# Kernel tuning notes

Measured on AMD Instinct MI355X. Metric: run time of the kernel, lower is better.

Reference implementation:

```python
import jax, jax.numpy as jnp
import numpy as np

B = 8192      # batch tokens
D = 2048      # d_model
N = 32768
K = 32        # top-k sparsity


def setup_inputs() -> dict:
    key = jax.random.key(0)
    k1, k2 = jax.random.split(key, 2)
    x = jax.random.normal(k1, (B, D), dtype=jnp.float32)
    # encoder weight [N, D] (nn.Linear(d_model, n_dirs).weight)
    enc_w = jax.random.normal(k2, (N, D), dtype=jnp.float32) * (1.0 / np.sqrt(D))
    # decoder initialized as encoder transpose, then unit-normed columns
    dec_w = enc_w.T  # [D, N]
    dec_w = dec_w / jnp.linalg.norm(dec_w, axis=0, keepdims=True)
    pre_bias = jnp.zeros((D,), dtype=jnp.float32)
    latent_bias = jnp.zeros((N,), dtype=jnp.float32)
    return {"x": x, "enc_w": enc_w, "dec_w": dec_w,
            "pre_bias": pre_bias, "latent_bias": latent_bias}


def reference(x, enc_w, dec_w, pre_bias, latent_bias):
    # latents_pre_act = (x - pre_bias) @ enc_w.T + latent_bias
    xc = x - pre_bias                                   # [B, D]
    latents = xc @ enc_w.T + latent_bias                # [B, N]
    # single-shard sharded_topk == plain top-k (sh_comm is None -> k_in = k)
    vals, inds = jax.lax.top_k(latents, K)              # [B, K]
    vals = jax.nn.relu(vals)
    # sparse decode: gather only the K active decoder columns per token
    cols = dec_w.T[inds]                                # [B, K, D]
    recons = jnp.einsum('bk,bkd->bd', vals, cols) + pre_bias  # [B, D]
    return recons
```

## Files before the change

### kernel.cpp

```cpp
#include <hip/hip_runtime.h>
#include <stdint.h>

#define B_TOK 8192
#define DMODEL 2048
#define NDIR 32768
#define KTOP 32
#define CAP 512
#define NREF 64
#define THRESH 2.5f

typedef __attribute__((ext_vector_type(8))) short short8;
typedef __attribute__((ext_vector_type(4))) float f32x4;

__device__ __forceinline__ uint16_t f2bf(float f) {
  uint32_t u = __float_as_uint(f);
  u = (u + 0x7fffu + ((u >> 16) & 1u)) >> 16;
  return (uint16_t)u;
}
__device__ __forceinline__ float bf2f(uint32_t u) { return __uint_as_float(u << 16); }

__device__ __forceinline__ void async_load16(const void* g, void* l) {
  __builtin_amdgcn_global_load_lds(
      (const __attribute__((address_space(1))) unsigned int*)g,
      (__attribute__((address_space(3))) unsigned int*)l, 16, 0, 0);
}

__global__ void prep_x_k(const float* __restrict__ x, const float* __restrict__ pre_bias,
                         uint16_t* __restrict__ xh) {
  size_t i = ((size_t)blockIdx.x * blockDim.x + threadIdx.x) * 4;
  float4 v = *reinterpret_cast<const float4*>(x + i);
  int d = (int)(i & (DMODEL - 1));
  float4 p = *reinterpret_cast<const float4*>(pre_bias + d);
  ushort4 o;
  o.x = f2bf(v.x - p.x); o.y = f2bf(v.y - p.y);
  o.z = f2bf(v.z - p.z); o.w = f2bf(v.w - p.w);
  *reinterpret_cast<ushort4*>(xh + i) = o;
}

__global__ void prep_w_k(const float* __restrict__ w, uint16_t* __restrict__ wh) {
  size_t i = ((size_t)blockIdx.x * blockDim.x + threadIdx.x) * 4;
  float4 v = *reinterpret_cast<const float4*>(w + i);
  ushort4 o;
  o.x = f2bf(v.x); o.y = f2bf(v.y); o.z = f2bf(v.z); o.w = f2bf(v.w);
  *reinterpret_cast<ushort4*>(wh + i) = o;
}

__global__ __launch_bounds__(512, 2) void gemm_topk(
    const uint16_t* __restrict__ xh, const uint16_t* __restrict__ wh,
    const float* __restrict__ latent_bias,
    float* __restrict__ cand_val, int* __restrict__ cand_idx, int* __restrict__ cand_cnt) {
  __shared__ char smem[131072];
  const int tid = threadIdx.x;
  const int w = tid >> 6, l = tid & 63;
  const int lr = l & 15, g = l >> 4;
  const int wm_w = (w >> 2) * 128;
  const int wn_w = (w & 3) * 64;

  int bid = blockIdx.x;
  int swz = (bid & 7) * 512 + (bid >> 3);
  const int bm = swz >> 7, bn = swz & 127;
  const int m0i = bm * 256, n0i = bn * 256;

  const char* Agb = (const char*)xh + (size_t)m0i * 4096;
  const char* Bgb = (const char*)wh + (size_t)n0i * 4096;

  const int key = (lr & 7) << 4;
  const int cx0 = (g << 4) ^ key;
  const int cx1 = (64 | (g << 4)) ^ key;

  const char* ArdBase = smem + (wm_w >> 7) * 16384;
  const char* BrdBase = smem + 32768 + (wn_w >> 7) * 16384;
  const int bhr = wn_w & 64;

  f32x4 acc[8][4] = {};
  short8 a[8], b[8];

  auto stage = [&](const char* grow0, char* dst) {
#pragma unroll
    for (int inst = 0; inst < 2; ++inst) {
      int o = inst * 8192 + tid * 16;
      int row = o >> 7;
      int cb = (o & 127) ^ ((row & 7) << 4);
      async_load16(grow0 + (size_t)row * 4096 + cb, dst + inst * 8192 + (tid >> 6) * 1024);
    }
  };

  const int NT = DMODEL / 64;

  stage(Agb, smem);
  stage(Agb + 524288, smem + 16384);
  stage(Bgb, smem + 32768);
  stage(Bgb + 524288, smem + 49152);
  stage(Bgb + 128, smem + 65536 + 32768);
  stage(Bgb + 524288 + 128, smem + 65536 + 49152);
  asm volatile("s_waitcnt vmcnt(4)" ::: "memory");
  __builtin_amdgcn_s_barrier();

  for (int t = 0; t < NT; ++t) {
    const int p = t & 1;
    const char* At = ArdBase + p * 65536;
    const char* Bt = BrdBase + p * 65536;
    char* SA = smem + ((t + 1) & 1) * 65536;
    char* SB = smem + p * 65536 + 32768;
    const char* Ag = Agb + (size_t)(t + 1) * 128;
    const char* Bg = Bgb + (size_t)(t + 2) * 128;
    const bool s1 = (t + 1 < NT), s2 = (t + 2 < NT);

#pragma unroll
    for (int f = 0; f < 4; ++f) {
      const char* rA = At + (f * 16 + lr) * 128;
      a[f * 2 + 0] = *(const short8*)(rA + cx0);
      a[f * 2 + 1] = *(const short8*)(rA + cx1);
    }
#pragma unroll
    for (int f = 0; f < 2; ++f) {
      const char* rB = Bt + (bhr + f * 16 + lr) * 128;
      b[f * 2 + 0] = *(const short8*)(rB + cx0);
      b[f * 2 + 1] = *(const short8*)(rB + cx1);
    }
    if (s1) stage(Ag, SA);
    __builtin_amdgcn_s_barrier();
    asm volatile("s_waitcnt lgkmcnt(0)" ::: "memory");
    __builtin_amdgcn_s_setprio(1);
#pragma unroll
    for (int fm = 0; fm < 4; ++fm)
#pragma unroll
      for (int fn = 0; fn < 2; ++fn)
#pragma unroll
        for (int kk = 0; kk < 2; ++kk)
          acc[fm][fn] = __builtin_amdgcn_mfma_f32_16x16x32_bf16(a[fm * 2 + kk], b[fn * 2 + kk],
                                                                acc[fm][fn], 0, 0, 0);
    __builtin_amdgcn_s_setprio(0);
    __builtin_amdgcn_s_barrier();

#pragma unroll
    for (int f = 2; f < 4; ++f) {
      const char* rB = Bt + (bhr + f * 16 + lr) * 128;
      b[f * 2 + 0] = *(const short8*)(rB + cx0);
      b[f * 2 + 1] = *(const short8*)(rB + cx1);
    }
    if (s1) stage(Ag + 524288, SA + 16384);
    __builtin_amdgcn_s_barrier();
    asm volatile("s_waitcnt lgkmcnt(0)" ::: "memory");
    __builtin_amdgcn_s_setprio(1);
#pragma unroll
    for (int fm = 0; fm < 4; ++fm)
#pragma unroll
      for (int fn = 2; fn < 4; ++fn)
#pragma unroll
        for (int kk = 0; kk < 2; ++kk)
          acc[fm][fn] = __builtin_amdgcn_mfma_f32_16x16x32_bf16(a[fm * 2 + kk], b[fn * 2 + kk],
                                                                acc[fm][fn], 0, 0, 0);
    __builtin_amdgcn_s_setprio(0);
    __builtin_amdgcn_s_barrier();

#pragma unroll
    for (int f = 0; f < 4; ++f) {
      const char* rA = At + ((f + 4) * 16 + lr) * 128;
      a[f * 2 + 0] = *(const short8*)(rA + cx0);
      a[f * 2 + 1] = *(const short8*)(rA + cx1);
    }
    if (s2) stage(Bg, SB);
    __builtin_amdgcn_s_barrier();
    asm volatile("s_waitcnt lgkmcnt(0)" ::: "memory");
    __builtin_amdgcn_s_setprio(1);
#pragma unroll
    for (int fm = 4; fm < 8; ++fm)
#pragma unroll
      for (int fn = 2; fn < 4; ++fn)
#pragma unroll
        for (int kk = 0; kk < 2; ++kk)
          acc[fm][fn] = __builtin_amdgcn_mfma_f32_16x16x32_bf16(a[(fm - 4) * 2 + kk],
                                                                b[fn * 2 + kk], acc[fm][fn], 0, 0, 0);
    __builtin_amdgcn_s_setprio(0);
    __builtin_amdgcn_s_barrier();

    if (s2) stage(Bg + 524288, SB + 16384);
    if (t < NT - 2)
      asm volatile("s_waitcnt vmcnt(4)" ::: "memory");
    else
      asm volatile("s_waitcnt vmcnt(0)" ::: "memory");
    __builtin_amdgcn_s_barrier();
    __builtin_amdgcn_s_setprio(1);
#pragma unroll
    for (int fm = 4; fm < 8; ++fm)
#pragma unroll
      for (int fn = 0; fn < 2; ++fn)
#pragma unroll
        for (int kk = 0; kk < 2; ++kk)
          acc[fm][fn] = __builtin_amdgcn_mfma_f32_16x16x32_bf16(a[(fm - 4) * 2 + kk],
                                                                b[fn * 2 + kk], acc[fm][fn], 0, 0, 0);
    __builtin_amdgcn_s_setprio(0);
    __builtin_amdgcn_s_barrier();
  }

#pragma unroll
  for (int fn = 0; fn < 4; ++fn) {
    int gn = n0i + wn_w + fn * 16 + lr;
    float lb = latent_bias[gn];
#pragma unroll
    for (int fm = 0; fm < 8; ++fm) {
      int gmb = m0i + wm_w + fm * 16 + g * 4;
#pragma unroll
      for (int j = 0; j < 4; ++j) {
        float v = acc[fm][fn][j] + lb;
        if (v > THRESH) {
          int gm = gmb + j;
          int pos = atomicAdd(&cand_cnt[gm], 1);
          if (pos < CAP) {
            cand_val[(size_t)gm * CAP + pos] = v;
            cand_idx[(size_t)gm * CAP + pos] = gn;
          }
        }
      }
    }
  }
}

__global__ __launch_bounds__(256) void select_refine(
    const float* __restrict__ x, const float* __restrict__ pre_bias,
    const float* __restrict__ enc_w, const float* __restrict__ latent_bias,
    const float* __restrict__ cand_val, const int* __restrict__ cand_idx,
    const int* __restrict__ cand_cnt,
    float* __restrict__ sel_val, int* __restrict__ sel_idx) {
  __shared__ float sv[CAP];
  __shared__ int si[CAP];
  __shared__ float xc[DMODEL];
  __shared__ double red[4];
  __shared__ double rv[NREF];
  __shared__ int ri[NREF];

  const int row = blockIdx.x, tid = threadIdx.x;

  for (int d = tid; d < DMODEL; d += 256)
    xc[d] = x[(size_t)row * DMODEL + d] - pre_bias[d];

  int c = cand_cnt[row];
  if (c > CAP) c = CAP;
  for (int i = tid; i < CAP; i += 256) {
    if (i < c) {
      sv[i] = cand_val[(size_t)row * CAP + i];
      si[i] = cand_idx[(size_t)row * CAP + i];
    } else {
      sv[i] = -1e30f;
      si[i] = 0x7fffffff;
    }
  }

  for (int k = 2; k <= CAP; k <<= 1) {
    for (int j = k >> 1; j > 0; j >>= 1) {
      __syncthreads();
      int i = ((tid & ~(j - 1)) << 1) | (tid & (j - 1));
      int p = i | j;
      bool up = ((i & k) == 0);
      float va = sv[i], vb = sv[p];
      int ia = si[i], ib = si[p];
      bool aFirst = (va > vb) || (va == vb && ia < ib);
      if (up ? (!aFirst) : aFirst) {
        sv[i] = vb; sv[p] = va; si[i] = ib; si[p] = ia;
      }
    }
  }
  __syncthreads();

  const int nref = c < NREF ? c : NREF;
  for (int jc = 0; jc < NREF; ++jc) {
    if (jc < nref) {
      int n = si[jc];
      const float* wrow = enc_w + (size_t)n * DMODEL;
      double s = 0.0;
      for (int d = tid; d < DMODEL; d += 256)
        s += (double)xc[d] * (double)wrow[d];
#pragma unroll
      for (int off = 32; off > 0; off >>= 1)
        s += __shfl_down(s, off);
      if ((tid & 63) == 0) red[tid >> 6] = s;
      __syncthreads();
      if (tid == 0) {
        rv[jc] = red[0] + red[1] + red[2] + red[3] + (double)latent_bias[n];
        ri[jc] = n;
      }
      __syncthreads();
    } else {
      if (tid == 0) { rv[jc] = -1e300; ri[jc] = 0x7fffffff; }
    }
  }
  __syncthreads();

  for (int k = 2; k <= NREF; k <<= 1) {
    for (int j = k >> 1; j > 0; j >>= 1) {
      __syncthreads();
      if (tid < NREF / 2) {
        int i = ((tid & ~(j - 1)) << 1) | (tid & (j - 1));
        int p = i | j;
        bool up = ((i & k) == 0);
        double va = rv[i], vb = rv[p];
        int ia = ri[i], ib = ri[p];
        bool aFirst = (va > vb) || (va == vb && ia < ib);
        if (up ? (!aFirst) : aFirst) {
          rv[i] = vb; rv[p] = va; ri[i] = ib; ri[p] = ia;
        }
      }
    }
  }
  __syncthreads();
  if (tid < KTOP) {
    double v = rv[tid];
    int n = ri[tid];
    float f = (n < NDIR && v > 0.0) ? (float)v : 0.0f;
    sel_val[(size_t)row * KTOP + tid] = f;
    sel_idx[(size_t)row * KTOP + tid] = (n < NDIR) ? n : 0;
  }
}

__global__ void transpose_dec(const float* __restrict__ dec_w, uint16_t* __restrict__ dec_wt) {
  __shared__ float tile[32][33];
  int n0 = blockIdx.x * 32, d0 = blockIdx.y * 32;
  int tx = threadIdx.x, ty = threadIdx.y;
#pragma unroll
  for (int i = 0; i < 4; ++i)
    tile[ty + i * 8][tx] = dec_w[(size_t)(d0 + ty + i * 8) * NDIR + n0 + tx];
  __syncthreads();
#pragma unroll
  for (int i = 0; i < 4; ++i)
    dec_wt[(size_t)(n0 + ty + i * 8) * DMODEL + d0 + tx] = f2bf(tile[tx][ty + i * 8]);
}

__global__ __launch_bounds__(256) void decode_k(
    const uint16_t* __restrict__ dec_wt, const float* __restrict__ sel_val,
    const int* __restrict__ sel_idx, const float* __restrict__ pre_bias,
    float* __restrict__ out) {
  __shared__ float vs[KTOP];
  __shared__ int isx[KTOP];
  const int b = blockIdx.x, tid = threadIdx.x;
  if (tid < KTOP) {
    vs[tid] = sel_val[(size_t)b * KTOP + tid];
    isx[tid] = sel_idx[(size_t)b * KTOP + tid];
  }
  __syncthreads();
  const int d = tid * 8;
  float acc[8];
  float4 p0 = *reinterpret_cast<const float4*>(pre_bias + d);
  float4 p1 = *reinterpret_cast<const float4*>(pre_bias + d + 4);
  acc[0] = p0.x; acc[1] = p0.y; acc[2] = p0.z; acc[3] = p0.w;
  acc[4] = p1.x; acc[5] = p1.y; acc[6] = p1.z; acc[7] = p1.w;
#pragma unroll 4
  for (int k = 0; k < KTOP; ++k) {
    float v = vs[k];
    int n = isx[k];
    uint4 raw = *reinterpret_cast<const uint4*>(dec_wt + (size_t)n * DMODEL + d);
    acc[0] += v * bf2f(raw.x & 0xffffu); acc[1] += v * bf2f(raw.x >> 16);
    acc[2] += v * bf2f(raw.y & 0xffffu); acc[3] += v * bf2f(raw.y >> 16);
    acc[4] += v * bf2f(raw.z & 0xffffu); acc[5] += v * bf2f(raw.z >> 16);
    acc[6] += v * bf2f(raw.w & 0xffffu); acc[7] += v * bf2f(raw.w >> 16);
  }
  float4 o0{acc[0], acc[1], acc[2], acc[3]};
  float4 o1{acc[4], acc[5], acc[6], acc[7]};
  *reinterpret_cast<float4*>(out + (size_t)b * DMODEL + d) = o0;
  *reinterpret_cast<float4*>(out + (size_t)b * DMODEL + d + 4) = o1;
}

extern "C" void kernel_launch(void* const* d_in, const int* in_sizes, int n_in,
                              void* d_out, int out_size, void* d_ws, size_t ws_size,
                              hipStream_t stream) {
  const float* x = (const float*)d_in[0];
  const float* enc_w = (const float*)d_in[1];
  const float* dec_w = (const float*)d_in[2];
  const float* pre_bias = (const float*)d_in[3];
  const float* latent_bias = (const float*)d_in[4];
  float* out = (float*)d_out;

  char* ws = (char*)d_ws;
  size_t off = 0;
  uint16_t* xh = (uint16_t*)(ws + off); off += (size_t)B_TOK * DMODEL * 2;
  uint16_t* wh = (uint16_t*)(ws + off); off += (size_t)NDIR * DMODEL * 2;
  uint16_t* dec_wt = (uint16_t*)(ws + off); off += (size_t)NDIR * DMODEL * 2;
  float* cand_val = (float*)(ws + off); off += (size_t)B_TOK * CAP * 4;
  int* cand_idx = (int*)(ws + off); off += (size_t)B_TOK * CAP * 4;
  int* cand_cnt = (int*)(ws + off); off += (size_t)B_TOK * 4;
  float* sel_val = (float*)(ws + off); off += (size_t)B_TOK * KTOP * 4;
  int* sel_idx = (int*)(ws + off); off += (size_t)B_TOK * KTOP * 4;
  (void)ws_size; (void)in_sizes; (void)n_in; (void)out_size;

  hipMemsetAsync(cand_cnt, 0, (size_t)B_TOK * 4, stream);

  prep_x_k<<<(B_TOK * DMODEL) / (256 * 4), 256, 0, stream>>>(x, pre_bias, xh);
  prep_w_k<<<(NDIR * DMODEL) / (256 * 4), 256, 0, stream>>>(enc_w, wh);
  transpose_dec<<<dim3(NDIR / 32, DMODEL / 32), dim3(32, 8), 0, stream>>>(dec_w, dec_wt);
  gemm_topk<<<(B_TOK / 256) * (NDIR / 256), 512, 0, stream>>>(
      xh, wh, latent_bias, cand_val, cand_idx, cand_cnt);
  select_refine<<<B_TOK, 256, 0, stream>>>(
      x, pre_bias, enc_w, latent_bias, cand_val, cand_idx, cand_cnt, sel_val, sel_idx);
  decode_k<<<B_TOK, 256, 0, stream>>>(dec_wt, sel_val, sel_idx, pre_bias, out);
}
```

Before: 2.333 ms.

## Prefetch next-tile LDS fragments and refine only near-boundary candidates per wave

The GEMM main loop splits its register fragments into A-low/A-high and B-P/B-Q sets and reorders the four MFMA quadrants. The next tile's first fragments are now loaded during the last quadrant, and the explicit lgkmcnt(0) waits are removed so LDS reads can overlap MFMA work. The select/refine kernel no longer recomputes the top 64 candidates in fp64 one at a time with block-wide syncs. It refines the top 32 plus up to 40 candidates whose bf16 score lies within a small band of the 32nd value, assigning one candidate per wave with no per-candidate barriers. The band heuristic risks missing true top-k members that fall outside the delta, and dropping the lgkmcnt waits relies on the compiler inserting the needed waits.

```diff
diff --git a/kernel.cpp b/kernel.cpp
--- a/kernel.cpp
+++ b/kernel.cpp
@@ -6,7 +6,8 @@
 #define NDIR 32768
 #define KTOP 32
 #define CAP 512
-#define NREF 64
+#define BANDCAP 40
+#define BAND_DELTA 0.06f
 #define THRESH 2.5f
 
 typedef __attribute__((ext_vector_type(8))) short short8;
@@ -73,7 +74,7 @@
   const int bhr = wn_w & 64;
 
   f32x4 acc[8][4] = {};
-  short8 a[8], b[8];
+  short8 aL[8], aH[8], bP[4], bQ[4];
 
   auto stage = [&](const char* grow0, char* dst) {
 #pragma unroll
@@ -95,6 +96,18 @@
   stage(Bgb + 524288 + 128, smem + 65536 + 49152);
   asm volatile("s_waitcnt vmcnt(4)" ::: "memory");
   __builtin_amdgcn_s_barrier();
+#pragma unroll
+  for (int f = 0; f < 4; ++f) {
+    const char* rA = ArdBase + (f * 16 + lr) * 128;
+    aL[f * 2 + 0] = *(const short8*)(rA + cx0);
+    aL[f * 2 + 1] = *(const short8*)(rA + cx1);
+  }
+#pragma unroll
+  for (int f = 0; f < 2; ++f) {
+    const char* rB = BrdBase + (bhr + f * 16 + lr) * 128;
+    bP[f * 2 + 0] = *(const short8*)(rB + cx0);
+    bP[f * 2 + 1] = *(const short8*)(rB + cx1);
+  }
 
   for (int t = 0; t < NT; ++t) {
     const int p = t & 1;
@@ -107,20 +120,13 @@
     const bool s1 = (t + 1 < NT), s2 = (t + 2 < NT);
 
 #pragma unroll
-    for (int f = 0; f < 4; ++f) {
-      const char* rA = At + (f * 16 + lr) * 128;
-      a[f * 2 + 0] = *(const short8*)(rA + cx0);
-      a[f * 2 + 1] = *(const short8*)(rA + cx1);
-    }
-#pragma unroll
     for (int f = 0; f < 2; ++f) {
-      const char* rB = Bt + (bhr + f * 16 + lr) * 128;
-      b[f * 2 + 0] = *(const short8*)(rB + cx0);
-      b[f * 2 + 1] = *(const short8*)(rB + cx1);
+      const char* rB = Bt + (bhr + (f + 2) * 16 + lr) * 128;
+      bQ[f * 2 + 0] = *(const short8*)(rB + cx0);
+      bQ[f * 2 + 1] = *(const short8*)(rB + cx1);
     }
     if (s1) stage(Ag, SA);
     __builtin_amdgcn_s_barrier();
-    asm volatile("s_waitcnt lgkmcnt(0)" ::: "memory");
     __builtin_amdgcn_s_setprio(1);
 #pragma unroll
     for (int fm = 0; fm < 4; ++fm)
@@ -128,20 +134,19 @@
       for (int fn = 0; fn < 2; ++fn)
 #pragma unroll
         for (int kk = 0; kk < 2; ++kk)
-          acc[fm][fn] = __builtin_amdgcn_mfma_f32_16x16x32_bf16(a[fm * 2 + kk], b[fn * 2 + kk],
+          acc[fm][fn] = __builtin_amdgcn_mfma_f32_16x16x32_bf16(aL[fm * 2 + kk], bP[fn * 2 + kk],
                                                                 acc[fm][fn], 0, 0, 0);
     __builtin_amdgcn_s_setprio(0);
     __builtin_amdgcn_s_barrier();
 
 #pragma unroll
-    for (int f = 2; f < 4; ++f) {
-      const char* rB = Bt + (bhr + f * 16 + lr) * 128;
-      b[f * 2 + 0] = *(const short8*)(rB + cx0);
-      b[f * 2 + 1] = *(const short8*)(rB + cx1);
+    for (int f = 0; f < 4; ++f) {
+      const char* rA = At + ((f + 4) * 16 + lr) * 128;
+      aH[f * 2 + 0] = *(const short8*)(rA + cx0);
+      aH[f * 2 + 1] = *(const short8*)(rA + cx1);
     }
     if (s1) stage(Ag + 524288, SA + 16384);
     __builtin_amdgcn_s_barrier();
-    asm volatile("s_waitcnt lgkmcnt(0)" ::: "memory");
     __builtin_amdgcn_s_setprio(1);
 #pragma unroll
     for (int fm = 0; fm < 4; ++fm)
@@ -149,29 +154,23 @@
       for (int fn = 2; fn < 4; ++fn)
 #pragma unroll
         for (int kk = 0; kk < 2; ++kk)
-          acc[fm][fn] = __builtin_amdgcn_mfma_f32_16x16x32_bf16(a[fm * 2 + kk], b[fn * 2 + kk],
+          acc[fm][fn] = __builtin_amdgcn_mfma_f32_16x16x32_bf16(aL[fm * 2 + kk],
+                                                                bQ[(fn - 2) * 2 + kk],
                                                                 acc[fm][fn], 0, 0, 0);
     __builtin_amdgcn_s_setprio(0);
     __builtin_amdgcn_s_barrier();
 
-#pragma unroll
-    for (int f = 0; f < 4; ++f) {
-      const char* rA = At + ((f + 4) * 16 + lr) * 128;
-      a[f * 2 + 0] = *(const short8*)(rA + cx0);
-      a[f * 2 + 1] = *(const short8*)(rA + cx1);
-    }
     if (s2) stage(Bg, SB);
     __builtin_amdgcn_s_barrier();
-    asm volatile("s_waitcnt lgkmcnt(0)" ::: "memory");
     __builtin_amdgcn_s_setprio(1);
 #pragma unroll
     for (int fm = 4; fm < 8; ++fm)
 #pragma unroll
-      for (int fn = 2; fn < 4; ++fn)
+      for (int fn = 0; fn < 2; ++fn)
 #pragma unroll
         for (int kk = 0; kk < 2; ++kk)
-          acc[fm][fn] = __builtin_amdgcn_mfma_f32_16x16x32_bf16(a[(fm - 4) * 2 + kk],
-                                                                b[fn * 2 + kk], acc[fm][fn], 0, 0, 0);
+          acc[fm][fn] = __builtin_amdgcn_mfma_f32_16x16x32_bf16(aH[(fm - 4) * 2 + kk],
+                                                                bP[fn * 2 + kk], acc[fm][fn], 0, 0, 0);
     __builtin_amdgcn_s_setprio(0);
     __builtin_amdgcn_s_barrier();
 
@@ -181,15 +180,32 @@
     else
       asm volatile("s_waitcnt vmcnt(0)" ::: "memory");
     __builtin_amdgcn_s_barrier();
+    if (t + 1 < NT) {
+      const char* An = ArdBase + ((t + 1) & 1) * 65536;
+      const char* Bn = BrdBase + ((t + 1) & 1) * 65536;
+#pragma unroll
+      for (int f = 0; f < 4; ++f) {
+        const char* rA = An + (f * 16 + lr) * 128;
+        aL[f * 2 + 0] = *(const short8*)(rA + cx0);
+        aL[f * 2 + 1] = *(const short8*)(rA + cx1);
+      }
+#pragma unroll
+      for (int f = 0; f < 2; ++f) {
+        const char* rB = Bn + (bhr + f * 16 + lr) * 128;
+        bP[f * 2 + 0] = *(const short8*)(rB + cx0);
+        bP[f * 2 + 1] = *(const short8*)(rB + cx1);
+      }
+    }
     __builtin_amdgcn_s_setprio(1);
 #pragma unroll
     for (int fm = 4; fm < 8; ++fm)
 #pragma unroll
-      for (int fn = 0; fn < 2; ++fn)
+      for (int fn = 2; fn < 4; ++fn)
 #pragma unroll
         for (int kk = 0; kk < 2; ++kk)
-          acc[fm][fn] = __builtin_amdgcn_mfma_f32_16x16x32_bf16(a[(fm - 4) * 2 + kk],
-                                                                b[fn * 2 + kk], acc[fm][fn], 0, 0, 0);
+          acc[fm][fn] = __builtin_amdgcn_mfma_f32_16x16x32_bf16(aH[(fm - 4) * 2 + kk],
+                                                                bQ[(fn - 2) * 2 + kk],
+                                                                acc[fm][fn], 0, 0, 0);
     __builtin_amdgcn_s_setprio(0);
     __builtin_amdgcn_s_barrier();
   }
@@ -226,14 +242,17 @@
   __shared__ float sv[CAP];
   __shared__ int si[CAP];
   __shared__ float xc[DMODEL];
-  __shared__ double red[4];
-  __shared__ double rv[NREF];
-  __shared__ int ri[NREF];
+  __shared__ double rall[128];
+  __shared__ int iall[128];
+  __shared__ int pext[BANDCAP];
+  __shared__ int nex;
 
   const int row = blockIdx.x, tid = threadIdx.x;
+  const int l = tid & 63, wv = tid >> 6;
 
   for (int d = tid; d < DMODEL; d += 256)
     xc[d] = x[(size_t)row * DMODEL + d] - pre_bias[d];
+  if (tid == 0) nex = 0;
 
   int c = cand_cnt[row];
   if (c > CAP) c = CAP;
@@ -263,50 +282,63 @@
   }
   __syncthreads();
 
-  const int nref = c < NREF ? c : NREF;
-  for (int jc = 0; jc < NREF; ++jc) {
-    if (jc < nref) {
-      int n = si[jc];
+  const float v32a = sv[31];
+  if (tid >= 32 && tid < 96) {
+    float v = sv[tid];
+    if (v > -1e29f && si[tid] < NDIR && fabsf(v - v32a) <= BAND_DELTA) {
+      int s = atomicAdd(&nex, 1);
+      if (s < BANDCAP) pext[s] = tid;
+    }
+  }
+  for (int e = tid; e < 128; e += 256) {
+    rall[e] = -1e300;
+    iall[e] = 0x7fffffff;
+  }
+  __syncthreads();
+
+  const int ne = nex < BANDCAP ? nex : BANDCAP;
+  const int nall = 32 + ne;
+  for (int e = wv; e < nall; e += 4) {
+    int pos = (e < 32) ? e : pext[e - 32];
+    int n = si[pos];
+    if (n < NDIR) {
       const float* wrow = enc_w + (size_t)n * DMODEL;
       double s = 0.0;
-      for (int d = tid; d < DMODEL; d += 256)
-        s += (double)xc[d] * (double)wrow[d];
+#pragma unroll
+      for (int u = 0; u < 32; ++u)
+        s += (double)xc[u * 64 + l] * (double)wrow[u * 64 + l];
 #pragma unroll
       for (int off = 32; off > 0; off >>= 1)
         s += __shfl_down(s, off);
-      if ((tid & 63) == 0) red[tid >> 6] = s;
-      __syncthreads();
-      if (tid == 0) {
-        rv[jc] = red[0] + red[1] + red[2] + red[3] + (double)latent_bias[n];
-        ri[jc] = n;
-      }
-      __syncthreads();
-    } else {
-      if (tid == 0) { rv[jc] = -1e300; ri[jc] = 0x7fffffff; }
-    }
-  }
-  __syncthreads();
-
-  for (int k = 2; k <= NREF; k <<= 1) {
+      if (l == 0) {
+        rall[e] = s + (double)latent_bias[n];
+        iall[e] = n;
+      }
+    }
+  }
+  __syncthreads();
+
+  for (int k = 2; k <= 128; k <<= 1) {
     for (int j = k >> 1; j > 0; j >>= 1) {
       __syncthreads();
-      if (tid < NREF / 2) {
+      if (tid < 64) {
         int i = ((tid & ~(j - 1)) << 1) | (tid & (j - 1));
         int p = i | j;
         bool up = ((i & k) == 0);
-        double va = rv[i], vb = rv[p];
-        int ia = ri[i], ib = ri[p];
+        double va = rall[i], vb = rall[p];
+        int ia = iall[i], ib = iall[p];
         bool aFirst = (va > vb) || (va == vb && ia < ib);
         if (up ? (!aFirst) : aFirst) {
-          rv[i] = vb; rv[p] = va; ri[i] = ib; ri[p] = ia;
+          rall[i] = vb; rall[p] = va; iall[i] = ib; iall[p] = ia;
         }
       }
     }
   }
   __syncthreads();
+
   if (tid < KTOP) {
-    double v = rv[tid];
-    int n = ri[tid];
+    double v = rall[tid];
+    int n = iall[tid];
     float f = (n < NDIR && v > 0.0) ? (float)v : 0.0f;
     sel_val[(size_t)row * KTOP + tid] = f;
     sel_idx[(size_t)row * KTOP + tid] = (n < NDIR) ? n : 0;
```

Result: faster. 1.999 ms (-14.3%).
